# Performance work log

Hardware: AMD Instinct MI355X
Metric: run time of the kernel (lower is better)

The kernel has to match this reference:

```python
import jax, jax.numpy as jnp
import numpy as np

K = 6            # kmer length
NF = 8192        # n_filters (> 4**K so kmer_params has shape (NF, 4, K))
M = 4 ** K       # 4096 kmers
B = 1024         # batch


def setup_inputs() -> dict:
    key = jax.random.key(0)
    k1, k2 = jax.random.split(key)
    freq = jax.random.uniform(k1, (B, M), dtype=jnp.float32)          # kmer frequencies (B, 4^k)
    kmer_params = jax.random.normal(k2, (NF, 4, K), dtype=jnp.float32)
    temperature = jnp.ones((1,), dtype=jnp.float32)
    # base-4 digits of arange(4^k), most-significant first == itertools.product order
    pos = 4 ** jnp.arange(K - 1, -1, -1)
    kmer_idcs = ((jnp.arange(M)[:, None] // pos[None, :]) % 4).astype(jnp.int32)  # (M, K)
    return {"freq": freq, "kmer_params": kmer_params,
            "temperature": temperature, "kmer_idcs": kmer_idcs}


def reference(freq, kmer_params, temperature, kmer_idcs):
    k = kmer_params.shape[-1]
    # matches[f, i] = sum_j kmer_params[f, kmer_idcs[i, j], j]
    # Advanced indexing broadcasts (M, k) indices against arange(k): result (F, M, k).
    # This replaces torch's expand-to-(F, M, 1, k) + gather + squeeze + sum(-1).
    matches = kmer_params[:, kmer_idcs, jnp.arange(k)].sum(axis=-1)   # (F, M)
    probs = jax.nn.softmax(matches / temperature, axis=1)             # softmax over kmers
    pooled = freq @ probs.T                                           # (B, F)
    profile = pooled / pooled.sum(axis=1, keepdims=True)
    return profile
```

## Files before the change

### kernel.cpp

```cpp
#include <hip/hip_runtime.h>


typedef __bf16  bf16x8 __attribute__((ext_vector_type(8)));
typedef float   f32x4  __attribute__((ext_vector_type(4)));

#define GLD16(gp, lp)                                                          \
  __builtin_amdgcn_global_load_lds(                                            \
      (const __attribute__((address_space(1))) void*)(gp),                     \
      (__attribute__((address_space(3))) void*)(lp), 16, 0, 0)

__device__ __forceinline__ short f2bf(float x) {
  unsigned u = __float_as_uint(x);
  unsigned r = (u + 0x7fffu + ((u >> 16) & 1u)) >> 16;
  return (short)r;
}

__device__ __forceinline__ float wave_max(float v) {
  #pragma unroll
  for (int off = 32; off; off >>= 1) v = fmaxf(v, __shfl_xor(v, off, 64));
  return v;
}
__device__ __forceinline__ float wave_sum(float v) {
  #pragma unroll
  for (int off = 32; off; off >>= 1) v += __shfl_xor(v, off, 64);
  return v;
}

__global__ __launch_bounds__(256) void prep_kernel(const float* __restrict__ freq,
                                                   const float* __restrict__ kp,
                                                   const float* __restrict__ temp,
                                                   short* __restrict__ freqb,
                                                   float* __restrict__ E1t,
                                                   float* __restrict__ E2) {
  __shared__ float E1loc[64][64];
  __shared__ float E2loc[64][64];
  const int blk = blockIdx.x;
  const int t = threadIdx.x;

  if (blk < 4096) {
    int idx = blk * 256 + t;
    float4 v = ((const float4*)freq)[idx];
    short4 o;
    o.x = f2bf(v.x); o.y = f2bf(v.y); o.z = f2bf(v.z); o.w = f2bf(v.w);
    ((short4*)freqb)[idx] = o;
    return;
  }

  const int bb = blk - 4096;
  const int f0 = bb * 64;
  const int lane = t & 63, wave = t >> 6;
  const float invT = 1.0f / temp[0];
  const int d0 = (lane >> 4) & 3, d1 = (lane >> 2) & 3, d2 = lane & 3;

  #pragma unroll
  for (int ffi = 0; ffi < 16; ffi++) {
    const int floc = wave * 16 + ffi;
    const float* P = kp + (size_t)(f0 + floc) * 24;
    const float thi = P[d0 * 6 + 0] + P[d1 * 6 + 1] + P[d2 * 6 + 2];
    const float tlo = P[d0 * 6 + 3] + P[d1 * 6 + 4] + P[d2 * 6 + 5];
    const float mxhi = wave_max(thi), mxlo = wave_max(tlo);
    const float e1 = __expf((thi - mxhi) * invT);
    const float e2 = __expf((tlo - mxlo) * invT);
    const float s1 = wave_sum(e1), s2 = wave_sum(e2);
    const float invZ = 1.0f / (s1 * s2);
    E1loc[floc][lane] = e1 * invZ;
    E2loc[floc][lane] = e2;
  }
  __syncthreads();

  {
    const int h = t >> 2, c0 = (t & 3) * 16;
    float tmp[16];
    #pragma unroll
    for (int cc = 0; cc < 16; cc++) tmp[cc] = E1loc[c0 + cc][h];
    float* dst = E1t + (size_t)h * 8192 + f0 + c0;
    #pragma unroll
    for (int q = 0; q < 4; q++)
      ((f32x4*)dst)[q] = (f32x4){tmp[q*4], tmp[q*4+1], tmp[q*4+2], tmp[q*4+3]};
  }

  {
    const int fl = t >> 2, l0 = (t & 3) * 16;
    float* dst = E2 + (size_t)(f0 + fl) * 64 + l0;
    #pragma unroll
    for (int q = 0; q < 4; q++)
      ((f32x4*)dst)[q] = *(const f32x4*)&E2loc[fl][l0 + q * 4];
  }
}

__global__ __launch_bounds__(256, 3) void gemm_kernel(const short* __restrict__ A,
                                                      const float* __restrict__ E1t,
                                                      const float* __restrict__ E2,
                                                      float* __restrict__ C) {
  __shared__ short As[64 * 256];

  const int t = threadIdx.x;
  const int lane = t & 63, wave = t >> 6;
  const int quad = lane >> 4, l16 = lane & 15;
  const int m0 = blockIdx.y * 64;
  const int n0 = blockIdx.x * 128;
  const int wn = wave * 32;

  f32x4 acc[4][2];
  #pragma unroll
  for (int i = 0; i < 4; i++)
    #pragma unroll
    for (int j = 0; j < 2; j++) acc[i][j] = (f32x4){0.f, 0.f, 0.f, 0.f};

  int nrow[2];
  #pragma unroll
  for (int j = 0; j < 2; j++) nrow[j] = n0 + wn + j * 16 + l16;

  float4 e2a[2][2], e2b[2][2];
  #pragma unroll
  for (int j = 0; j < 2; j++)
    #pragma unroll
    for (int par = 0; par < 2; par++) {
      const float* p = E2 + (size_t)nrow[j] * 64 + par * 32 + quad * 8;
      e2a[j][par] = *(const float4*)p;
      e2b[j][par] = *(const float4*)(p + 4);
    }

  const int lrow_half = lane >> 5;
  const int pblk = lane & 31;
  const int sw = l16 & 7;

  for (int kt = 0; kt < 16; kt++) {
    const int kofs = kt * 256;

    float e1v[2][4];
    #pragma unroll
    for (int hh = 0; hh < 4; hh++)
      #pragma unroll
      for (int j = 0; j < 2; j++)
        e1v[j][hh] = E1t[(kt * 4 + hh) * 8192 + nrow[j]];

    __syncthreads();
    #pragma unroll
    for (int c = 0; c < 8; c++) {
      const int chunk = wave * 8 + c;
      const int row = chunk * 2 + lrow_half;
      const int src_col = (pblk ^ (row & 7)) * 8;
      GLD16(A + (m0 + row) * 4096 + kofs + src_col, &As[chunk * 512 + lane * 8]);
    }
    __syncthreads();

    #pragma unroll
    for (int ks = 0; ks < 8; ks++) {
      const int q = ks * 4 + quad;
      const int pcol = (q ^ sw) * 8;
      bf16x8 a[4];
      #pragma unroll
      for (int i = 0; i < 4; i++)
        a[i] = *(const bf16x8*)&As[(i * 16 + l16) * 256 + pcol];

      const int hh = ks >> 1, par = ks & 1;
      bf16x8 b[2];
      #pragma unroll
      for (int j = 0; j < 2; j++) {
        const float s = e1v[j][hh];
        bf16x8 bb;
        bb[0] = (__bf16)(s * e2a[j][par].x);
        bb[1] = (__bf16)(s * e2a[j][par].y);
        bb[2] = (__bf16)(s * e2a[j][par].z);
        bb[3] = (__bf16)(s * e2a[j][par].w);
        bb[4] = (__bf16)(s * e2b[j][par].x);
        bb[5] = (__bf16)(s * e2b[j][par].y);
        bb[6] = (__bf16)(s * e2b[j][par].z);
        bb[7] = (__bf16)(s * e2b[j][par].w);
        b[j] = bb;
      }

      #pragma unroll
      for (int i = 0; i < 4; i++)
        #pragma unroll
        for (int j = 0; j < 2; j++)
          acc[i][j] = __builtin_amdgcn_mfma_f32_16x16x32_bf16(a[i], b[j], acc[i][j], 0, 0, 0);
    }
  }

  #pragma unroll
  for (int i = 0; i < 4; i++) {
    #pragma unroll
    for (int r = 0; r < 4; r++) {
      const int brow = m0 + i * 16 + quad * 4 + r;
      float* crow = C + (size_t)brow * 8192 + n0 + wn + l16;
      #pragma unroll
      for (int j = 0; j < 2; j++) crow[j * 16] = acc[i][j][r];
    }
  }
}

__global__ __launch_bounds__(256) void norm_kernel(float* __restrict__ out) {
  const int b = blockIdx.x;
  const int t = threadIdx.x;
  const int lane = t & 63, wave = t >> 6;
  __shared__ float red[4];

  float4* row = (float4*)(out + (size_t)b * 8192);
  float4 v[8];
  float s = 0.0f;
  #pragma unroll
  for (int q = 0; q < 8; q++) {
    v[q] = row[q * 256 + t];
    s += (v[q].x + v[q].y) + (v[q].z + v[q].w);
  }
  float ws = wave_sum(s);
  if (lane == 0) red[wave] = ws;
  __syncthreads();
  float tot = (red[0] + red[1]) + (red[2] + red[3]);
  float inv = 1.0f / tot;
  #pragma unroll
  for (int q = 0; q < 8; q++) {
    v[q].x *= inv; v[q].y *= inv; v[q].z *= inv; v[q].w *= inv;
    row[q * 256 + t] = v[q];
  }
}

extern "C" void kernel_launch(void* const* d_in, const int* in_sizes, int n_in,
                              void* d_out, int out_size, void* d_ws, size_t ws_size,
                              hipStream_t stream) {
  const float* freq    = (const float*)d_in[0];
  const float* kparams = (const float*)d_in[1];
  const float* temp    = (const float*)d_in[2];

  float* out = (float*)d_out;

  short* freqb = (short*)d_ws;
  float* E1t   = (float*)(freqb + (size_t)1024 * 4096);
  float* E2    = E1t + (size_t)64 * 8192;

  prep_kernel<<<4224, 256, 0, stream>>>(freq, kparams, temp, freqb, E1t, E2);
  gemm_kernel<<<dim3(64, 16), 256, 0, stream>>>(freqb, E1t, E2, out);
  norm_kernel<<<1024, 256, 0, stream>>>(out);
}
```

Before: 181.2 us.

## Keep E2 fragments in registers and apply E1 scale after MFMA per k-group

The GEMM kernel now loads each 64-wide E2 block once into bf16 register fragments. For each of the 64 high-digit groups it runs two MFMAs against freq loaded directly from global memory into registers, then scales the partial tile by E1 and accumulates in fp32. This removes the LDS staging, the block barriers, and the per-step scale-and-convert of B fragments. The cost is scalar FMAs after every MFMA pair, accumulators restarted from zero each group, and uncoalesced direct global loads of A rows without LDS reuse across waves.

Result: slower. 206.1 us (+13.7%).

```diff
diff --git a/kernel.cpp b/kernel.cpp
--- a/kernel.cpp
+++ b/kernel.cpp
@@ -3,11 +3,6 @@
 
 typedef __bf16  bf16x8 __attribute__((ext_vector_type(8)));
 typedef float   f32x4  __attribute__((ext_vector_type(4)));
-
-#define GLD16(gp, lp)                                                          \
-  __builtin_amdgcn_global_load_lds(                                            \
-      (const __attribute__((address_space(1))) void*)(gp),                     \
-      (__attribute__((address_space(3))) void*)(lp), 16, 0, 0)
 
 __device__ __forceinline__ short f2bf(float x) {
   unsigned u = __float_as_uint(x);
@@ -78,7 +73,6 @@
     for (int q = 0; q < 4; q++)
       ((f32x4*)dst)[q] = (f32x4){tmp[q*4], tmp[q*4+1], tmp[q*4+2], tmp[q*4+3]};
   }
-
   {
     const int fl = t >> 2, l0 = (t & 3) * 16;
     float* dst = E2 + (size_t)(f0 + fl) * 64 + l0;
@@ -92,102 +86,69 @@
                                                       const float* __restrict__ E1t,
                                                       const float* __restrict__ E2,
                                                       float* __restrict__ C) {
-  __shared__ short As[64 * 256];
-
   const int t = threadIdx.x;
   const int lane = t & 63, wave = t >> 6;
   const int quad = lane >> 4, l16 = lane & 15;
-  const int m0 = blockIdx.y * 64;
   const int n0 = blockIdx.x * 128;
-  const int wn = wave * 32;
+  const int mw = blockIdx.y * 64 + wave * 16;
 
-  f32x4 acc[4][2];
+  bf16x8 bfr[8][2];
   #pragma unroll
-  for (int i = 0; i < 4; i++)
+  for (int j = 0; j < 8; j++)
     #pragma unroll
-    for (int j = 0; j < 2; j++) acc[i][j] = (f32x4){0.f, 0.f, 0.f, 0.f};
-
-  int nrow[2];
-  #pragma unroll
-  for (int j = 0; j < 2; j++) nrow[j] = n0 + wn + j * 16 + l16;
-
-  float4 e2a[2][2], e2b[2][2];
-  #pragma unroll
-  for (int j = 0; j < 2; j++)
-    #pragma unroll
-    for (int par = 0; par < 2; par++) {
-      const float* p = E2 + (size_t)nrow[j] * 64 + par * 32 + quad * 8;
-      e2a[j][par] = *(const float4*)p;
-      e2b[j][par] = *(const float4*)(p + 4);
+    for (int ks = 0; ks < 2; ks++) {
+      const float* p = E2 + (size_t)(n0 + j * 16 + l16) * 64 + ks * 32 + quad * 8;
+      float4 lo = *(const float4*)p;
+      float4 hi = *(const float4*)(p + 4);
+      bf16x8 bb;
+      bb[0] = (__bf16)lo.x; bb[1] = (__bf16)lo.y; bb[2] = (__bf16)lo.z; bb[3] = (__bf16)lo.w;
+      bb[4] = (__bf16)hi.x; bb[5] = (__bf16)hi.y; bb[6] = (__bf16)hi.z; bb[7] = (__bf16)hi.w;
+      bfr[j][ks] = bb;
     }
 
-  const int lrow_half = lane >> 5;
-  const int pblk = lane & 31;
-  const int sw = l16 & 7;
+  f32x4 acc[8];
+  #pragma unroll
+  for (int j = 0; j < 8; j++) acc[j] = (f32x4){0.f, 0.f, 0.f, 0.f};
+  const f32x4 zf = (f32x4){0.f, 0.f, 0.f, 0.f};
 
-  for (int kt = 0; kt < 16; kt++) {
-    const int kofs = kt * 256;
+  const short* Arow  = A + (size_t)(mw + l16) * 4096 + quad * 8;
+  const float* E1b   = E1t + n0 + l16;
 
-    float e1v[2][4];
+  bf16x8 a0 = *(const bf16x8*)(Arow);
+  bf16x8 a1 = *(const bf16x8*)(Arow + 32);
+  float e1v[8];
+  #pragma unroll
+  for (int j = 0; j < 8; j++) e1v[j] = E1b[j * 16];
+
+  for (int kt = 0; kt < 64; kt++) {
+    const int ktn = (kt < 63) ? kt + 1 : 63;
+    bf16x8 na0 = *(const bf16x8*)(Arow + ktn * 64);
+    bf16x8 na1 = *(const bf16x8*)(Arow + ktn * 64 + 32);
+    float ne1[8];
     #pragma unroll
-    for (int hh = 0; hh < 4; hh++)
-      #pragma unroll
-      for (int j = 0; j < 2; j++)
-        e1v[j][hh] = E1t[(kt * 4 + hh) * 8192 + nrow[j]];
-
-    __syncthreads();
-    #pragma unroll
-    for (int c = 0; c < 8; c++) {
-      const int chunk = wave * 8 + c;
-      const int row = chunk * 2 + lrow_half;
-      const int src_col = (pblk ^ (row & 7)) * 8;
-      GLD16(A + (m0 + row) * 4096 + kofs + src_col, &As[chunk * 512 + lane * 8]);
-    }
-    __syncthreads();
+    for (int j = 0; j < 8; j++) ne1[j] = E1b[(size_t)ktn * 8192 + j * 16];
 
     #pragma unroll
-    for (int ks = 0; ks < 8; ks++) {
-      const int q = ks * 4 + quad;
-      const int pcol = (q ^ sw) * 8;
-      bf16x8 a[4];
-      #pragma unroll
-      for (int i = 0; i < 4; i++)
-        a[i] = *(const bf16x8*)&As[(i * 16 + l16) * 256 + pcol];
+    for (int j = 0; j < 8; j++) {
+      f32x4 P = __builtin_amdgcn_mfma_f32_16x16x32_bf16(a0, bfr[j][0], zf, 0, 0, 0);
+      P = __builtin_amdgcn_mfma_f32_16x16x32_bf16(a1, bfr[j][1], P, 0, 0, 0);
+      const float s = e1v[j];
+      acc[j][0] += s * P[0];
+      acc[j][1] += s * P[1];
+      acc[j][2] += s * P[2];
+      acc[j][3] += s * P[3];
+    }
 
-      const int hh = ks >> 1, par = ks & 1;
-      bf16x8 b[2];
-      #pragma unroll
-      for (int j = 0; j < 2; j++) {
-        const float s = e1v[j][hh];
-        bf16x8 bb;
-        bb[0] = (__bf16)(s * e2a[j][par].x);
-        bb[1] = (__bf16)(s * e2a[j][par].y);
-        bb[2] = (__bf16)(s * e2a[j][par].z);
-        bb[3] = (__bf16)(s * e2a[j][par].w);
-        bb[4] = (__bf16)(s * e2b[j][par].x);
-        bb[5] = (__bf16)(s * e2b[j][par].y);
-        bb[6] = (__bf16)(s * e2b[j][par].z);
-        bb[7] = (__bf16)(s * e2b[j][par].w);
-        b[j] = bb;
-      }
-
-      #pragma unroll
-      for (int i = 0; i < 4; i++)
-        #pragma unroll
-        for (int j = 0; j < 2; j++)
-          acc[i][j] = __builtin_amdgcn_mfma_f32_16x16x32_bf16(a[i], b[j], acc[i][j], 0, 0, 0);
-    }
+    a0 = na0; a1 = na1;
+    #pragma unroll
+    for (int j = 0; j < 8; j++) e1v[j] = ne1[j];
   }
 
   #pragma unroll
-  for (int i = 0; i < 4; i++) {
+  for (int r = 0; r < 4; r++) {
+    float* crow = C + (size_t)(mw + quad * 4 + r) * 8192 + n0 + l16;
     #pragma unroll
-    for (int r = 0; r < 4; r++) {
-      const int brow = m0 + i * 16 + quad * 4 + r;
-      float* crow = C + (size_t)brow * 8192 + n0 + wn + l16;
-      #pragma unroll
-      for (int j = 0; j < 2; j++) crow[j * 16] = acc[i][j][r];
-    }
+    for (int j = 0; j < 8; j++) crow[j * 16] = acc[j][r];
   }
 }
 
```
